# Kernel optimization log

Hardware: AMD Instinct MI355X
Metric: run time of the kernel (lower is better)

The kernel has to match this reference:

```python
import jax, jax.numpy as jnp
import numpy as np

ALPHA = 0.2          # LeakyReLU negative slope (args.alpha)
NEG_INF = -9e15      # zero_vec constant from the torch source


def _build_mask(neighbors):
    """Faithful port of A_creat: scatter-add edge counts, row-normalize,
    add self-loops (identity), row-normalize again. neighbors: [N, deg] int."""
    N, deg = neighbors.shape
    rows = jnp.repeat(jnp.arange(N), deg)
    counts = jnp.zeros((N, N), jnp.float32).at[rows, neighbors.reshape(-1)].add(1.0)
    m = counts / counts.sum(axis=1, keepdims=True)
    m = m + jnp.eye(N, dtype=jnp.float32)
    m = m / m.sum(axis=1, keepdims=True)
    return m


def setup_inputs() -> dict:
    key = jax.random.key(0)
    k1, k2, k3, k4 = jax.random.split(key, 4)
    N, F_IN, F_OUT, DEG = 8192, 256, 128, 32
    h = jax.random.normal(k1, (N, F_IN), dtype=jnp.float32)
    neighbors = jax.random.randint(k2, (N, DEG), 0, N)
    # torch uses nn.init.uniform_ (U[0,1)) for both W and a
    W = jax.random.uniform(k3, (F_IN, F_OUT), dtype=jnp.float32)
    a = jax.random.uniform(k4, (2 * F_OUT, 1), dtype=jnp.float32)
    return {"h": h, "W": W, "a": a, "neighbors": neighbors}


def reference(h, W, a, neighbors):
    F_out = W.shape[1]
    mask = _build_mask(neighbors)                 # [N, N]
    hW = h @ W                                    # [N, F_out]
    h1 = hW @ a[:F_out]                           # [N, 1]
    h2 = hW @ a[F_out:]                           # [N, 1]
    e = mask * (h1 + h2.T)                        # dense masked additive scores
    e = jnp.where(e > 0, e, ALPHA * e)            # LeakyReLU
    att = jnp.where(e != 0.0, e, NEG_INF)         # mask out zeros
    att = jax.nn.softmax(att, axis=1)             # row softmax (dropout off in eval)
    feat = att @ hW                               # aggregate
    return jax.nn.elu(feat)
```

## Files before the change

### kernel.cpp

```cpp
#include <hip/hip_runtime.h>
#include <math.h>

#define N_NODES 8192
#define F_IN    256
#define F_OUT   128
#define DEG     32
#define ALPHA   0.2f

typedef __attribute__((ext_vector_type(8))) short short8;
typedef __attribute__((ext_vector_type(4))) float floatx4;

__device__ __forceinline__ unsigned short f2bf(float x) {
    unsigned u = __float_as_uint(x);
    return (unsigned short)((u + 0x7fffu + ((u >> 16) & 1u)) >> 16);
}

__global__ __launch_bounds__(64) void pack_w_kernel(
        const float* __restrict__ W, unsigned short* __restrict__ Wtf) {
    const int lane = threadIdx.x;
    const int quad = lane >> 4;
    const int l15  = lane & 15;
    const int kt   = blockIdx.x >> 3;
    const int gnt  = blockIdx.x & 7;
    const int n    = gnt * 16 + l15;
    const int kb   = kt * 32 + quad * 8;

    unsigned short s[8];
    #pragma unroll
    for (int j = 0; j < 8; ++j)
        s[j] = f2bf(W[(size_t)(kb + j) * F_OUT + n]);

    uint4 p;
    p.x = (unsigned)s[0] | ((unsigned)s[1] << 16);
    p.y = (unsigned)s[2] | ((unsigned)s[3] << 16);
    p.z = (unsigned)s[4] | ((unsigned)s[5] << 16);
    p.w = (unsigned)s[6] | ((unsigned)s[7] << 16);
    ((uint4*)Wtf)[(size_t)blockIdx.x * 64 + lane] = p;
}

__global__ __launch_bounds__(64) void wa_kernel(
        const float* __restrict__ W, const float* __restrict__ a,
        float* __restrict__ wa1, float* __restrict__ wa2) {
    const int k = blockIdx.x * 64 + threadIdx.x;
    const float* wr = W + (size_t)k * F_OUT;
    float s1 = 0.f, s2 = 0.f;
    #pragma unroll 4
    for (int n = 0; n < F_OUT; n += 4) {
        float4 wv = *(const float4*)(wr + n);
        float4 a1 = *(const float4*)(a + n);
        float4 a2 = *(const float4*)(a + F_OUT + n);
        s1 = fmaf(wv.x, a1.x, fmaf(wv.y, a1.y, fmaf(wv.z, a1.z, fmaf(wv.w, a1.w, s1))));
        s2 = fmaf(wv.x, a2.x, fmaf(wv.y, a2.y, fmaf(wv.z, a2.z, fmaf(wv.w, a2.w, s2))));
    }
    wa1[k] = s1;
    wa2[k] = s2;
}

__global__ __launch_bounds__(256) void gemm_mfma_v6(
        const float* __restrict__ h,
        const unsigned short* __restrict__ Wtf,
        const float* __restrict__ wa1,
        const float* __restrict__ wa2,
        unsigned short* __restrict__ hWb,
        float* __restrict__ h1,
        float* __restrict__ h2) {
    const int tid  = threadIdx.x;
    const int wave = tid >> 6;
    const int lane = tid & 63;
    const int quad = lane >> 4;
    const int l15  = lane & 15;
    const int row0 = blockIdx.x * 16;

    const float* hrow = h + (size_t)(row0 + l15) * F_IN + quad * 8;
    const short8* Wf  = (const short8*)Wtf;

    floatx4 acc[2] = {{0.f,0.f,0.f,0.f},{0.f,0.f,0.f,0.f}};
    float s1 = 0.f, s2 = 0.f;

    #pragma unroll
    for (int kt = 0; kt < 8; ++kt) {
        float4 v0 = *(const float4*)(hrow + kt * 32);
        float4 v1 = *(const float4*)(hrow + kt * 32 + 4);
        short8 af;
        af[0] = (short)f2bf(v0.x); af[1] = (short)f2bf(v0.y);
        af[2] = (short)f2bf(v0.z); af[3] = (short)f2bf(v0.w);
        af[4] = (short)f2bf(v1.x); af[5] = (short)f2bf(v1.y);
        af[6] = (short)f2bf(v1.z); af[7] = (short)f2bf(v1.w);

        #pragma unroll
        for (int nt = 0; nt < 2; ++nt) {
            short8 bf = Wf[(size_t)(kt * 8 + wave * 2 + nt) * 64 + lane];
            acc[nt] = __builtin_amdgcn_mfma_f32_16x16x32_bf16(af, bf, acc[nt], 0, 0, 0);
        }

        if (wave == 0) {
            const int kb = kt * 32 + quad * 8;
            float4 u0 = *(const float4*)(wa1 + kb);
            float4 u1 = *(const float4*)(wa1 + kb + 4);
            float4 t0 = *(const float4*)(wa2 + kb);
            float4 t1 = *(const float4*)(wa2 + kb + 4);
            s1 = fmaf(v0.x,u0.x, fmaf(v0.y,u0.y, fmaf(v0.z,u0.z, fmaf(v0.w,u0.w, s1))));
            s1 = fmaf(v1.x,u1.x, fmaf(v1.y,u1.y, fmaf(v1.z,u1.z, fmaf(v1.w,u1.w, s1))));
            s2 = fmaf(v0.x,t0.x, fmaf(v0.y,t0.y, fmaf(v0.z,t0.z, fmaf(v0.w,t0.w, s2))));
            s2 = fmaf(v1.x,t1.x, fmaf(v1.y,t1.y, fmaf(v1.z,t1.z, fmaf(v1.w,t1.w, s2))));
        }
    }

    #pragma unroll
    for (int nt = 0; nt < 2; ++nt) {
        const int col = wave * 32 + nt * 16 + l15;
        #pragma unroll
        for (int reg = 0; reg < 4; ++reg) {
            const int row = row0 + quad * 4 + reg;
            hWb[(size_t)row * F_OUT + col] = f2bf(acc[nt][reg]);
        }
    }

    if (wave == 0) {
        s1 += __shfl_xor(s1, 16); s1 += __shfl_xor(s1, 32);
        s2 += __shfl_xor(s2, 16); s2 += __shfl_xor(s2, 32);
        if (lane < 16) {
            h1[row0 + l15] = s1;
            h2[row0 + l15] = s2;
        }
    }
}

__global__ __launch_bounds__(256) void attn_kernel(
        const unsigned int* __restrict__ hWb,
        const float* __restrict__ h1,
        const float* __restrict__ h2,
        const int*   __restrict__ nbr,
        float* __restrict__ out) {
    const int wave = threadIdx.x >> 6;
    const int lane = threadIdx.x & 63;
    const int row  = blockIdx.x * 4 + wave;

    int col = -1;
    if (lane < DEG)       col = nbr[(size_t)row * DEG + lane];
    else if (lane == DEG) col = row;

    int cnt = 0;
    int firstq = lane;
    #pragma unroll
    for (int q = 0; q <= DEG; ++q) {
        int cq = __shfl(col, q);
        bool same = (cq == col);
        if (same && q < DEG)    cnt++;
        if (same && q < firstq) firstq = q;
    }
    const bool active = (lane <= DEG) && (col >= 0) && (firstq == lane);

    float mask_val = (float)cnt * (1.0f / 64.0f) + ((col == row) ? 0.5f : 0.0f);

    const float h1row = h1[row];
    float h2c = active ? h2[col] : 0.f;
    float s = mask_val * (h1row + h2c);
    float e = (s > 0.f) ? s : ALPHA * s;
    bool valid = active && (e != 0.0f);

    float ev = valid ? e : -INFINITY;
    #pragma unroll
    for (int off = 32; off > 0; off >>= 1)
        ev = fmaxf(ev, __shfl_xor(ev, off));
    float w = valid ? __expf(e - ev) : 0.f;
    float denom = w;
    #pragma unroll
    for (int off = 32; off > 0; off >>= 1)
        denom += __shfl_xor(denom, off);
    float att = w / denom;

    float acc0 = 0.f, acc1 = 0.f;
    #pragma unroll
    for (int q = 0; q <= DEG; ++q) {
        float aq = __shfl(att, q);
        int   cq = __shfl(col, q);
        if (aq > 0.f) {
            unsigned v = hWb[(size_t)cq * (F_OUT / 2) + lane];
            float lo = __uint_as_float(v << 16);
            float hi = __uint_as_float(v & 0xffff0000u);
            acc0 = fmaf(aq, lo, acc0);
            acc1 = fmaf(aq, hi, acc1);
        }
    }

    float o0 = (acc0 > 0.f) ? acc0 : expm1f(acc0);
    float o1 = (acc1 > 0.f) ? acc1 : expm1f(acc1);
    *(float2*)(out + (size_t)row * F_OUT + 2 * lane) = make_float2(o0, o1);
}

extern "C" void kernel_launch(void* const* d_in, const int* in_sizes, int n_in,
                              void* d_out, int out_size, void* d_ws, size_t ws_size,
                              hipStream_t stream) {
    const float* h   = (const float*)d_in[0];
    const float* W   = (const float*)d_in[1];
    const float* a   = (const float*)d_in[2];
    const int*   nbr = (const int*)  d_in[3];
    float* out = (float*)d_out;

    unsigned short* hWb = (unsigned short*)d_ws;
    float* h1 = (float*)(hWb + (size_t)N_NODES * F_OUT);
    float* h2 = h1 + N_NODES;
    unsigned short* Wtf = (unsigned short*)(h2 + N_NODES);
    float* wa1 = (float*)(Wtf + (size_t)F_IN * F_OUT);
    float* wa2 = wa1 + F_IN;

    pack_w_kernel<<<64, 64, 0, stream>>>(W, Wtf);
    wa_kernel    <<<4,  64, 0, stream>>>(W, a, wa1, wa2);
    gemm_mfma_v6 <<<N_NODES / 16, 256, 0, stream>>>(h, Wtf, wa1, wa2, hWb, h1, h2);
    attn_kernel  <<<N_NODES / 4,  256, 0, stream>>>((const unsigned int*)hWb,
                                                    h1, h2, nbr, out);
}
```

Baseline: 94.04 us.

## Fuse GEMM and attention into a cooperative kernel with grid sync

Merges the two small weight-prep kernels into one launch and fuses the bf16 MFMA projection GEMM with the neighbor attention aggregation in a single cooperative kernel of 512 blocks separated by a grid-wide barrier. Each block computes 16 rows of hW, then after the grid sync handles 16 attention rows (4 per wave). This removes two kernel launches and the gaps between them. In exchange, the grid barrier adds its own cost, and only 512 blocks run, so parallelism per phase is lower than in the original 2048-block attention launch.

```diff
diff --git a/kernel.cpp b/kernel.cpp
--- a/kernel.cpp
+++ b/kernel.cpp
@@ -1,11 +1,16 @@
 #include <hip/hip_runtime.h>
+#include <hip/hip_cooperative_groups.h>
 #include <math.h>
+
+namespace cg = cooperative_groups;
 
 #define N_NODES 8192
 #define F_IN    256
 #define F_OUT   128
 #define DEG     32
 #define ALPHA   0.2f
+#define GBLK    512
+#define RPB     16
 
 typedef __attribute__((ext_vector_type(8))) short short8;
 typedef __attribute__((ext_vector_type(4))) float floatx4;
@@ -15,178 +20,181 @@
     return (unsigned short)((u + 0x7fffu + ((u >> 16) & 1u)) >> 16);
 }
 
-__global__ __launch_bounds__(64) void pack_w_kernel(
-        const float* __restrict__ W, unsigned short* __restrict__ Wtf) {
-    const int lane = threadIdx.x;
-    const int quad = lane >> 4;
-    const int l15  = lane & 15;
-    const int kt   = blockIdx.x >> 3;
-    const int gnt  = blockIdx.x & 7;
-    const int n    = gnt * 16 + l15;
-    const int kb   = kt * 32 + quad * 8;
-
-    unsigned short s[8];
-    #pragma unroll
-    for (int j = 0; j < 8; ++j)
-        s[j] = f2bf(W[(size_t)(kb + j) * F_OUT + n]);
-
-    uint4 p;
-    p.x = (unsigned)s[0] | ((unsigned)s[1] << 16);
-    p.y = (unsigned)s[2] | ((unsigned)s[3] << 16);
-    p.z = (unsigned)s[4] | ((unsigned)s[5] << 16);
-    p.w = (unsigned)s[6] | ((unsigned)s[7] << 16);
-    ((uint4*)Wtf)[(size_t)blockIdx.x * 64 + lane] = p;
-}
-
-__global__ __launch_bounds__(64) void wa_kernel(
+__global__ __launch_bounds__(64) void prep_kernel(
         const float* __restrict__ W, const float* __restrict__ a,
+        unsigned short* __restrict__ Wtf,
         float* __restrict__ wa1, float* __restrict__ wa2) {
-    const int k = blockIdx.x * 64 + threadIdx.x;
-    const float* wr = W + (size_t)k * F_OUT;
-    float s1 = 0.f, s2 = 0.f;
-    #pragma unroll 4
-    for (int n = 0; n < F_OUT; n += 4) {
-        float4 wv = *(const float4*)(wr + n);
-        float4 a1 = *(const float4*)(a + n);
-        float4 a2 = *(const float4*)(a + F_OUT + n);
-        s1 = fmaf(wv.x, a1.x, fmaf(wv.y, a1.y, fmaf(wv.z, a1.z, fmaf(wv.w, a1.w, s1))));
-        s2 = fmaf(wv.x, a2.x, fmaf(wv.y, a2.y, fmaf(wv.z, a2.z, fmaf(wv.w, a2.w, s2))));
+    const int bid = blockIdx.x;
+    const int tid = threadIdx.x;
+    if (bid < 64) {
+        const int quad = tid >> 4;
+        const int l15  = tid & 15;
+        const int kt   = bid >> 3;
+        const int gnt  = bid & 7;
+        const int n    = gnt * 16 + l15;
+        const int kb   = kt * 32 + quad * 8;
+        unsigned short s[8];
+        #pragma unroll
+        for (int j = 0; j < 8; ++j)
+            s[j] = f2bf(W[(size_t)(kb + j) * F_OUT + n]);
+        uint4 p;
+        p.x = (unsigned)s[0] | ((unsigned)s[1] << 16);
+        p.y = (unsigned)s[2] | ((unsigned)s[3] << 16);
+        p.z = (unsigned)s[4] | ((unsigned)s[5] << 16);
+        p.w = (unsigned)s[6] | ((unsigned)s[7] << 16);
+        ((uint4*)Wtf)[(size_t)bid * 64 + tid] = p;
+    } else {
+        const int k = (bid - 64) * 64 + tid;
+        const float* wr = W + (size_t)k * F_OUT;
+        float s1 = 0.f, s2 = 0.f;
+        #pragma unroll 4
+        for (int n = 0; n < F_OUT; n += 4) {
+            float4 wv = *(const float4*)(wr + n);
+            float4 a1 = *(const float4*)(a + n);
+            float4 a2 = *(const float4*)(a + F_OUT + n);
+            s1 = fmaf(wv.x,a1.x, fmaf(wv.y,a1.y, fmaf(wv.z,a1.z, fmaf(wv.w,a1.w, s1))));
+            s2 = fmaf(wv.x,a2.x, fmaf(wv.y,a2.y, fmaf(wv.z,a2.z, fmaf(wv.w,a2.w, s2))));
+        }
+        wa1[k] = s1;
+        wa2[k] = s2;
     }
-    wa1[k] = s1;
-    wa2[k] = s2;
-}
-
-__global__ __launch_bounds__(256) void gemm_mfma_v6(
+}
+
+__global__ __launch_bounds__(256) void fused_coop(
         const float* __restrict__ h,
         const unsigned short* __restrict__ Wtf,
         const float* __restrict__ wa1,
         const float* __restrict__ wa2,
+        const int*   __restrict__ nbr,
         unsigned short* __restrict__ hWb,
         float* __restrict__ h1,
-        float* __restrict__ h2) {
+        float* __restrict__ h2,
+        float* __restrict__ out) {
+    cg::grid_group grid = cg::this_grid();
+
     const int tid  = threadIdx.x;
     const int wave = tid >> 6;
     const int lane = tid & 63;
     const int quad = lane >> 4;
     const int l15  = lane & 15;
-    const int row0 = blockIdx.x * 16;
-
-    const float* hrow = h + (size_t)(row0 + l15) * F_IN + quad * 8;
-    const short8* Wf  = (const short8*)Wtf;
-
-    floatx4 acc[2] = {{0.f,0.f,0.f,0.f},{0.f,0.f,0.f,0.f}};
-    float s1 = 0.f, s2 = 0.f;
-
+    const int row0 = blockIdx.x * RPB;
+
+    {
+        const float* hrow = h + (size_t)(row0 + l15) * F_IN + quad * 8;
+        const short8* Wf  = (const short8*)Wtf;
+
+        floatx4 acc[2] = {{0.f,0.f,0.f,0.f},{0.f,0.f,0.f,0.f}};
+        float s1 = 0.f, s2 = 0.f;
+
+        #pragma unroll
+        for (int kt = 0; kt < 8; ++kt) {
+            float4 v0 = *(const float4*)(hrow + kt * 32);
+            float4 v1 = *(const float4*)(hrow + kt * 32 + 4);
+            short8 af;
+            af[0] = (short)f2bf(v0.x); af[1] = (short)f2bf(v0.y);
+            af[2] = (short)f2bf(v0.z); af[3] = (short)f2bf(v0.w);
+            af[4] = (short)f2bf(v1.x); af[5] = (short)f2bf(v1.y);
+            af[6] = (short)f2bf(v1.z); af[7] = (short)f2bf(v1.w);
+
+            #pragma unroll
+            for (int nt = 0; nt < 2; ++nt) {
+                short8 bf = Wf[(size_t)(kt * 8 + wave * 2 + nt) * 64 + lane];
+                acc[nt] = __builtin_amdgcn_mfma_f32_16x16x32_bf16(af, bf, acc[nt], 0, 0, 0);
+            }
+
+            if (wave == 0) {
+                const int kb = kt * 32 + quad * 8;
+                float4 u0 = *(const float4*)(wa1 + kb);
+                float4 u1 = *(const float4*)(wa1 + kb + 4);
+                float4 t0 = *(const float4*)(wa2 + kb);
+                float4 t1 = *(const float4*)(wa2 + kb + 4);
+                s1 = fmaf(v0.x,u0.x, fmaf(v0.y,u0.y, fmaf(v0.z,u0.z, fmaf(v0.w,u0.w, s1))));
+                s1 = fmaf(v1.x,u1.x, fmaf(v1.y,u1.y, fmaf(v1.z,u1.z, fmaf(v1.w,u1.w, s1))));
+                s2 = fmaf(v0.x,t0.x, fmaf(v0.y,t0.y, fmaf(v0.z,t0.z, fmaf(v0.w,t0.w, s2))));
+                s2 = fmaf(v1.x,t1.x, fmaf(v1.y,t1.y, fmaf(v1.z,t1.z, fmaf(v1.w,t1.w, s2))));
+            }
+        }
+
+        #pragma unroll
+        for (int nt = 0; nt < 2; ++nt) {
+            const int col = wave * 32 + nt * 16 + l15;
+            #pragma unroll
+            for (int reg = 0; reg < 4; ++reg) {
+                const int row = row0 + quad * 4 + reg;
+                hWb[(size_t)row * F_OUT + col] = f2bf(acc[nt][reg]);
+            }
+        }
+
+        if (wave == 0) {
+            s1 += __shfl_xor(s1, 16); s1 += __shfl_xor(s1, 32);
+            s2 += __shfl_xor(s2, 16); s2 += __shfl_xor(s2, 32);
+            if (lane < 16) {
+                h1[row0 + l15] = s1;
+                h2[row0 + l15] = s2;
+            }
+        }
+    }
+
+    __threadfence();
+    grid.sync();
+
+    const unsigned int* hWp = (const unsigned int*)hWb;
     #pragma unroll
-    for (int kt = 0; kt < 8; ++kt) {
-        float4 v0 = *(const float4*)(hrow + kt * 32);
-        float4 v1 = *(const float4*)(hrow + kt * 32 + 4);
-        short8 af;
-        af[0] = (short)f2bf(v0.x); af[1] = (short)f2bf(v0.y);
-        af[2] = (short)f2bf(v0.z); af[3] = (short)f2bf(v0.w);
-        af[4] = (short)f2bf(v1.x); af[5] = (short)f2bf(v1.y);
-        af[6] = (short)f2bf(v1.z); af[7] = (short)f2bf(v1.w);
-
-        #pragma unroll
-        for (int nt = 0; nt < 2; ++nt) {
-            short8 bf = Wf[(size_t)(kt * 8 + wave * 2 + nt) * 64 + lane];
-            acc[nt] = __builtin_amdgcn_mfma_f32_16x16x32_bf16(af, bf, acc[nt], 0, 0, 0);
-        }
-
-        if (wave == 0) {
-            const int kb = kt * 32 + quad * 8;
-            float4 u0 = *(const float4*)(wa1 + kb);
-            float4 u1 = *(const float4*)(wa1 + kb + 4);
-            float4 t0 = *(const float4*)(wa2 + kb);
-            float4 t1 = *(const float4*)(wa2 + kb + 4);
-            s1 = fmaf(v0.x,u0.x, fmaf(v0.y,u0.y, fmaf(v0.z,u0.z, fmaf(v0.w,u0.w, s1))));
-            s1 = fmaf(v1.x,u1.x, fmaf(v1.y,u1.y, fmaf(v1.z,u1.z, fmaf(v1.w,u1.w, s1))));
-            s2 = fmaf(v0.x,t0.x, fmaf(v0.y,t0.y, fmaf(v0.z,t0.z, fmaf(v0.w,t0.w, s2))));
-            s2 = fmaf(v1.x,t1.x, fmaf(v1.y,t1.y, fmaf(v1.z,t1.z, fmaf(v1.w,t1.w, s2))));
-        }
+    for (int r = 0; r < 4; ++r) {
+        const int row = row0 + wave * 4 + r;
+
+        int col = -1;
+        if (lane < DEG)       col = nbr[(size_t)row * DEG + lane];
+        else if (lane == DEG) col = row;
+
+        int cnt = 0;
+        int firstq = lane;
+        #pragma unroll
+        for (int q = 0; q <= DEG; ++q) {
+            int cq = __shfl(col, q);
+            bool same = (cq == col);
+            if (same && q < DEG)    cnt++;
+            if (same && q < firstq) firstq = q;
+        }
+        const bool active = (lane <= DEG) && (col >= 0) && (firstq == lane);
+
+        float mask_val = (float)cnt * (1.0f / 64.0f) + ((col == row) ? 0.5f : 0.0f);
+
+        const float h1row = h1[row];
+        float h2c = active ? h2[col] : 0.f;
+        float s = mask_val * (h1row + h2c);
+        float e = (s > 0.f) ? s : ALPHA * s;
+        bool valid = active && (e != 0.0f);
+
+        float ev = valid ? e : -INFINITY;
+        #pragma unroll
+        for (int off = 32; off > 0; off >>= 1)
+            ev = fmaxf(ev, __shfl_xor(ev, off));
+        float w = valid ? __expf(e - ev) : 0.f;
+        float denom = w;
+        #pragma unroll
+        for (int off = 32; off > 0; off >>= 1)
+            denom += __shfl_xor(denom, off);
+        float att = w / denom;
+
+        float acc0 = 0.f, acc1 = 0.f;
+        #pragma unroll
+        for (int q = 0; q <= DEG; ++q) {
+            float aq = __shfl(att, q);
+            int   cq = __shfl(col, q);
+            if (aq > 0.f) {
+                unsigned v = hWp[(size_t)cq * (F_OUT / 2) + lane];
+                float lo = __uint_as_float(v << 16);
+                float hi = __uint_as_float(v & 0xffff0000u);
+                acc0 = fmaf(aq, lo, acc0);
+                acc1 = fmaf(aq, hi, acc1);
+            }
+        }
+
+        float o0 = (acc0 > 0.f) ? acc0 : expm1f(acc0);
+        float o1 = (acc1 > 0.f) ? acc1 : expm1f(acc1);
+        *(float2*)(out + (size_t)row * F_OUT + 2 * lane) = make_float2(o0, o1);
     }
-
-    #pragma unroll
-    for (int nt = 0; nt < 2; ++nt) {
-        const int col = wave * 32 + nt * 16 + l15;
-        #pragma unroll
-        for (int reg = 0; reg < 4; ++reg) {
-            const int row = row0 + quad * 4 + reg;
-            hWb[(size_t)row * F_OUT + col] = f2bf(acc[nt][reg]);
-        }
-    }
-
-    if (wave == 0) {
-        s1 += __shfl_xor(s1, 16); s1 += __shfl_xor(s1, 32);
-        s2 += __shfl_xor(s2, 16); s2 += __shfl_xor(s2, 32);
-        if (lane < 16) {
-            h1[row0 + l15] = s1;
-            h2[row0 + l15] = s2;
-        }
-    }
-}
-
-__global__ __launch_bounds__(256) void attn_kernel(
-        const unsigned int* __restrict__ hWb,
-        const float* __restrict__ h1,
-        const float* __restrict__ h2,
-        const int*   __restrict__ nbr,
-        float* __restrict__ out) {
-    const int wave = threadIdx.x >> 6;
-    const int lane = threadIdx.x & 63;
-    const int row  = blockIdx.x * 4 + wave;
-
-    int col = -1;
-    if (lane < DEG)       col = nbr[(size_t)row * DEG + lane];
-    else if (lane == DEG) col = row;
-
-    int cnt = 0;
-    int firstq = lane;
-    #pragma unroll
-    for (int q = 0; q <= DEG; ++q) {
-        int cq = __shfl(col, q);
-        bool same = (cq == col);
-        if (same && q < DEG)    cnt++;
-        if (same && q < firstq) firstq = q;
-    }
-    const bool active = (lane <= DEG) && (col >= 0) && (firstq == lane);
-
-    float mask_val = (float)cnt * (1.0f / 64.0f) + ((col == row) ? 0.5f : 0.0f);
-
-    const float h1row = h1[row];
-    float h2c = active ? h2[col] : 0.f;
-    float s = mask_val * (h1row + h2c);
-    float e = (s > 0.f) ? s : ALPHA * s;
-    bool valid = active && (e != 0.0f);
-
-    float ev = valid ? e : -INFINITY;
-    #pragma unroll
-    for (int off = 32; off > 0; off >>= 1)
-        ev = fmaxf(ev, __shfl_xor(ev, off));
-    float w = valid ? __expf(e - ev) : 0.f;
-    float denom = w;
-    #pragma unroll
-    for (int off = 32; off > 0; off >>= 1)
-        denom += __shfl_xor(denom, off);
-    float att = w / denom;
-
-    float acc0 = 0.f, acc1 = 0.f;
-    #pragma unroll
-    for (int q = 0; q <= DEG; ++q) {
-        float aq = __shfl(att, q);
-        int   cq = __shfl(col, q);
-        if (aq > 0.f) {
-            unsigned v = hWb[(size_t)cq * (F_OUT / 2) + lane];
-            float lo = __uint_as_float(v << 16);
-            float hi = __uint_as_float(v & 0xffff0000u);
-            acc0 = fmaf(aq, lo, acc0);
-            acc1 = fmaf(aq, hi, acc1);
-        }
-    }
-
-    float o0 = (acc0 > 0.f) ? acc0 : expm1f(acc0);
-    float o1 = (acc1 > 0.f) ? acc1 : expm1f(acc1);
-    *(float2*)(out + (size_t)row * F_OUT + 2 * lane) = make_float2(o0, o1);
 }
 
 extern "C" void kernel_launch(void* const* d_in, const int* in_sizes, int n_in,
@@ -205,9 +213,11 @@
     float* wa1 = (float*)(Wtf + (size_t)F_IN * F_OUT);
     float* wa2 = wa1 + F_IN;
 
-    pack_w_kernel<<<64, 64, 0, stream>>>(W, Wtf);
-    wa_kernel    <<<4,  64, 0, stream>>>(W, a, wa1, wa2);
-    gemm_mfma_v6 <<<N_NODES / 16, 256, 0, stream>>>(h, Wtf, wa1, wa2, hWb, h1, h2);
-    attn_kernel  <<<N_NODES / 4,  256, 0, stream>>>((const unsigned int*)hWb,
-                                                    h1, h2, nbr, out);
-}
+    prep_kernel<<<68, 64, 0, stream>>>(W, a, Wtf, wa1, wa2);
+
+    void* kargs[] = {(void*)&h, (void*)&Wtf, (void*)&wa1, (void*)&wa2,
+                     (void*)&nbr, (void*)&hWb, (void*)&h1, (void*)&h2,
+                     (void*)&out};
+    hipLaunchCooperativeKernel((void*)fused_coop, dim3(GBLK), dim3(256),
+                               kargs, 0, stream);
+}
```

Result: slower. 253.2 us (+169.3%).
